# Kernel optimization log

Measured on AMD Instinct MI355X. Metric: run time of the kernel, lower is better.

The kernel has to match this reference:

```python
import jax, jax.numpy as jnp
import numpy as np
import math

AVGF = 16  # num_submatrices
TK = 4     # num_blocks
HA = 16    # num_heads
M = 2048   # M_size1 = C1*C2 = 32*64
DH = M // HA
EPS = 1e-5


def _layernorm(y, g, b):
    m = y.mean(-1, keepdims=True)
    v = ((y - m) ** 2).mean(-1, keepdims=True)
    return (y - m) / jnp.sqrt(v + EPS) * g + b


def setup_inputs() -> dict:
    key = jax.random.key(0)
    ks = jax.random.split(key, 10)
    f32 = jnp.float32
    return {
        "x": jax.random.normal(ks[0], (64, 32, 160), dtype=f32),
        "weight": jax.random.normal(ks[1], (M, M), dtype=f32),
        "bias": 0.02 * jax.random.normal(ks[2], (AVGF + 1, M), dtype=f32),
        "cls": 0.02 * jax.random.normal(ks[3], (1, M), dtype=f32),
        "Wqkv": jax.random.normal(ks[4], (TK, 3, HA, DH, M), dtype=f32),
        "Wo": jax.random.normal(ks[5], (TK, M, M), dtype=f32),
        "ln1_g": jnp.ones((M,), f32), "ln1_b": jnp.zeros((M,), f32),
        "ln2_g": jnp.ones((M,), f32), "ln2_b": jnp.zeros((M,), f32),
        "ln3_g": jnp.ones((M,), f32), "ln3_b": jnp.zeros((M,), f32),
        "fc1_w": jax.random.normal(ks[6], (4 * M, M), dtype=f32) * 0.02,
        "fc1_b": jnp.zeros((4 * M,), f32),
        "fc2_w": jax.random.normal(ks[7], (M, 4 * M), dtype=f32) * 0.02,
        "fc2_b": jnp.zeros((M,), f32),
    }


def reference(x, weight, bias, cls, Wqkv, Wo, ln1_g, ln1_b, ln2_g, ln2_b,
              ln3_g, ln3_b, fc1_w, fc1_b, fc2_w, fc2_b):
    inp = jnp.transpose(x, (2, 1, 0))           # [T, C1, C2] = [160, 32, 64]
    T, C1, C2 = inp.shape
    seg = T // AVGF
    # segment-average then flatten: [avgf, M]
    altx = inp.reshape(AVGF, seg, C1 * C2).mean(axis=1)
    savespace = jnp.einsum('lm,im->il', weight, altx)     # [avgf, M]
    savespace = jnp.concatenate([cls, savespace], axis=0) + bias  # [avgf+1, M]
    scale = 1.0 / math.sqrt(DH)

    def block(ss, params):
        Wqkv_a, Wo_a = params
        qkv = jnp.einsum('xhdm,im->xihd', Wqkv_a, _layernorm(ss, ln1_g, ln1_b))
        q, k, v = qkv[0], qkv[1], qkv[2]        # [avgf+1, hA, Dh]
        rsa = jnp.einsum('ihd,ihd->ih', q * scale, k)
        imv = rsa[..., None] * v                # [avgf+1, hA, Dh]
        # original loop: subj in 1..avgf-1  => cumsum over rows 0..avgf-1,
        # last row (index avgf) left untouched
        imv = jnp.concatenate([jnp.cumsum(imv[:AVGF], axis=0), imv[AVGF:]], axis=0)
        ss = imv.reshape(AVGF + 1, M) @ Wo_a.T + ss
        h = _layernorm(ss, ln2_g, ln2_b)
        h = jax.nn.gelu(h @ fc1_w.T + fc1_b, approximate=False) @ fc2_w.T + fc2_b
        return h + ss, None

    savespace, _ = jax.lax.scan(block, savespace, (Wqkv, Wo))
    out = _layernorm(savespace, ln3_g, ln3_b)
    return out.reshape(AVGF + 1, C1, C2)
```

## Files before the change

kernel.cpp:

```cpp
#include <hip/hip_runtime.h>
#include <math.h>


__global__ void k0_init(const float* __restrict__ x,
                        const float* __restrict__ bias,
                        const float* __restrict__ cls,
                        float* __restrict__ ss,
                        float* __restrict__ altx) {
    int idx = blockIdx.x * 256 + threadIdx.x;
    if (idx < 17 * 2048) {
        int r = idx >> 11, m = idx & 2047;
        float v = bias[idx];
        if (r == 0) v += cls[m];
        ss[idx] = v;
    }
    if (idx < 16 * 2048) {
        int i = idx >> 11, m = idx & 2047;
        int c1 = m >> 6, c2 = m & 63;
        const float* p = x + (size_t)(c2 * 32 + c1) * 160 + i * 10;
        float s = 0.f;
#pragma unroll
        for (int j = 0; j < 10; ++j) s += p[j];
        altx[idx] = s * 0.1f;
    }
}

template <int NR>
__global__ __launch_bounds__(256) void gemmS(
    const float* __restrict__ W, const float* __restrict__ act,
    float* __restrict__ P, int L, int K) {
    const int lane = threadIdx.x & 63;
    const int wv = threadIdx.x >> 6;
    const int l0 = blockIdx.x * 16 + wv * 4;
    const int slab = K / gridDim.y;
    const int k0 = blockIdx.y * slab;

    float acc[NR][4];
#pragma unroll
    for (int i = 0; i < NR; ++i)
#pragma unroll
        for (int r = 0; r < 4; ++r) acc[i][r] = 0.f;

    const float* Wp = W + (size_t)l0 * K + k0;
    const float* Ap = act + k0;

    for (int kk = 0; kk < slab; kk += 256) {
        const int idx = kk + lane * 4;
        const float4 w40 = *reinterpret_cast<const float4*>(Wp + idx);
        const float4 w41 = *reinterpret_cast<const float4*>(Wp + (size_t)K + idx);
        const float4 w42 = *reinterpret_cast<const float4*>(Wp + (size_t)2 * K + idx);
        const float4 w43 = *reinterpret_cast<const float4*>(Wp + (size_t)3 * K + idx);
#pragma unroll
        for (int i = 0; i < NR; ++i) {
            const float4 a4 = *reinterpret_cast<const float4*>(Ap + (size_t)i * K + idx);
            acc[i][0] += a4.x * w40.x + a4.y * w40.y + a4.z * w40.z + a4.w * w40.w;
            acc[i][1] += a4.x * w41.x + a4.y * w41.y + a4.z * w41.z + a4.w * w41.w;
            acc[i][2] += a4.x * w42.x + a4.y * w42.y + a4.z * w42.z + a4.w * w42.w;
            acc[i][3] += a4.x * w43.x + a4.y * w43.y + a4.z * w43.z + a4.w * w43.w;
        }
    }
    float vout = 0.f, vout2 = 0.f;
#pragma unroll
    for (int i = 0; i < NR; ++i)
#pragma unroll
        for (int r = 0; r < 4; ++r) {
            float v = acc[i][r];
#pragma unroll
            for (int off = 32; off; off >>= 1) v += __shfl_xor(v, off);
            if (i < 16) { if (lane == i * 4 + r) vout = v; }
            else        { if (lane == r)         vout2 = v; }
        }
    size_t pb = (size_t)blockIdx.y * NR * L + l0;
    P[pb + (size_t)(lane >> 2) * L + (lane & 3)] = vout;
    if (NR > 16 && lane < 4) P[pb + (size_t)16 * L + lane] = vout2;
}

__global__ void red_plain(const float* __restrict__ P, float* __restrict__ out,
                          int S, int NRL) {
    int idx = blockIdx.x * 256 + threadIdx.x;
    float s = 0.f;
    for (int y = 0; y < S; ++y) s += P[(size_t)y * NRL + idx];
    out[idx] = s;
}

__global__ void red_gelu(const float* __restrict__ P, const float* __restrict__ fb,
                         float* __restrict__ out, int S, int NRL) {
    int idx = blockIdx.x * 256 + threadIdx.x;
    float s = fb[idx & 8191];
    for (int y = 0; y < S; ++y) s += P[(size_t)y * NRL + idx];
    out[idx] = 0.5f * s * (1.f + erff(s * 0.70710678f));
}

__global__ void redln(const float* __restrict__ P, int S, int rowoff, int NRL,
                      const float* __restrict__ fb, float* __restrict__ ss,
                      const float* __restrict__ g, const float* __restrict__ b,
                      float* __restrict__ lnout) {
    const int row = blockIdx.x;
    const int tid = threadIdx.x;
    const int base = row * 2048;
    float vv[8];
    float s = 0.f, q = 0.f;
#pragma unroll
    for (int c = 0; c < 8; ++c) {
        int col = tid + c * 256;
        float xv = ss[base + col];
        if (row >= rowoff) {
            const float* pp = P + (size_t)(row - rowoff) * 2048 + col;
            for (int y = 0; y < S; ++y) xv += pp[(size_t)y * NRL];
        }
        if (fb != nullptr) xv += fb[col];
        ss[base + col] = xv;
        vv[c] = xv;
        s += xv;
        q += xv * xv;
    }
#pragma unroll
    for (int off = 32; off; off >>= 1) {
        s += __shfl_xor(s, off);
        q += __shfl_xor(q, off);
    }
    __shared__ float red[8];
    int wv = tid >> 6;
    if ((tid & 63) == 0) { red[wv] = s; red[4 + wv] = q; }
    __syncthreads();
    s = red[0] + red[1] + red[2] + red[3];
    q = red[4] + red[5] + red[6] + red[7];
    float mean = s * (1.f / 2048.f);
    float var = q * (1.f / 2048.f) - mean * mean;
    float rstd = rsqrtf(var + 1e-5f);
#pragma unroll
    for (int c = 0; c < 8; ++c) {
        int col = tid + c * 256;
        lnout[base + col] = (vv[c] - mean) * rstd * g[col] + b[col];
    }
}

__global__ void attn_kernel(const float* __restrict__ qkv, float* __restrict__ imv) {
    int h = blockIdx.x, lane = threadIdx.x;
    const float scale = 0.08838834764831845f;
    float run0 = 0.f, run1 = 0.f;
    for (int i = 0; i < 17; ++i) {
        const float* base = qkv + (size_t)i * 6144 + h * 128;
        float q0 = base[lane], q1 = base[lane + 64];
        float k0 = base[2048 + lane], k1 = base[2048 + lane + 64];
        float v0 = base[4096 + lane], v1 = base[4096 + lane + 64];
        float p = q0 * k0 + q1 * k1;
#pragma unroll
        for (int off = 32; off; off >>= 1) p += __shfl_xor(p, off);
        float rsa = p * scale;
        float iv0 = rsa * v0, iv1 = rsa * v1;
        float o0, o1;
        if (i < 16) { run0 += iv0; run1 += iv1; o0 = run0; o1 = run1; }
        else        { o0 = iv0; o1 = iv1; }
        imv[(size_t)i * 2048 + h * 128 + lane] = o0;
        imv[(size_t)i * 2048 + h * 128 + lane + 64] = o1;
    }
}

extern "C" void kernel_launch(void* const* d_in, const int* in_sizes, int n_in,
                              void* d_out, int out_size, void* d_ws, size_t ws_size,
                              hipStream_t stream) {
    const float* x      = (const float*)d_in[0];
    const float* weight = (const float*)d_in[1];
    const float* bias   = (const float*)d_in[2];
    const float* cls    = (const float*)d_in[3];
    const float* Wqkv   = (const float*)d_in[4];
    const float* Wo     = (const float*)d_in[5];
    const float* ln1_g  = (const float*)d_in[6];
    const float* ln1_b  = (const float*)d_in[7];
    const float* ln2_g  = (const float*)d_in[8];
    const float* ln2_b  = (const float*)d_in[9];
    const float* ln3_g  = (const float*)d_in[10];
    const float* ln3_b  = (const float*)d_in[11];
    const float* fc1_w  = (const float*)d_in[12];
    const float* fc1_b  = (const float*)d_in[13];
    const float* fc2_w  = (const float*)d_in[14];
    const float* fc2_b  = (const float*)d_in[15];
    float* out = (float*)d_out;

    float* ws     = (float*)d_ws;
    float* ss     = ws;
    float* altx   = ws + 34816;
    float* qkv    = ws + 67584;
    float* imv    = ws + 172032;
    float* tbuf   = ws + 206848;
    float* ln1buf = ws + 346112;
    float* ln2buf = ws + 380928;
    float* P      = ws + 415744;

    k0_init<<<136, 256, 0, stream>>>(x, bias, cls, ss, altx);
    gemmS<16><<<dim3(128, 4), 256, 0, stream>>>(weight, altx, P, 2048, 2048);
    redln<<<17, 256, 0, stream>>>(P, 4, 1, 32768, nullptr, ss, ln1_g, ln1_b, ln1buf);

    for (int k = 0; k < 4; ++k) {
        gemmS<17><<<dim3(384, 2), 256, 0, stream>>>(
            Wqkv + (size_t)k * 12582912, ln1buf, P, 6144, 2048);
        red_plain<<<408, 256, 0, stream>>>(P, qkv, 2, 104448);
        attn_kernel<<<16, 64, 0, stream>>>(qkv, imv);
        gemmS<17><<<dim3(128, 4), 256, 0, stream>>>(
            Wo + (size_t)k * 4194304, imv, P, 2048, 2048);
        redln<<<17, 256, 0, stream>>>(P, 4, 0, 34816, nullptr, ss, ln2_g, ln2_b, ln2buf);
        gemmS<17><<<dim3(512, 2), 256, 0, stream>>>(fc1_w, ln2buf, P, 8192, 2048);
        red_gelu<<<544, 256, 0, stream>>>(P, fc1_b, tbuf, 2, 139264);
        gemmS<17><<<dim3(128, 8), 256, 0, stream>>>(fc2_w, tbuf, P, 2048, 8192);
        if (k < 3)
            redln<<<17, 256, 0, stream>>>(P, 8, 0, 34816, fc2_b, ss, ln1_g, ln1_b, ln1buf);
        else
            redln<<<17, 256, 0, stream>>>(P, 8, 0, 34816, fc2_b, ss, ln3_g, ln3_b, out);
    }
}
```

Measured before the change: 580.7 us.

## Fuse layernorm, split-K reductions and GELU into GEMM activation staging

```diff
diff --git a/kernel.cpp b/kernel.cpp
--- a/kernel.cpp
+++ b/kernel.cpp
@@ -25,76 +25,98 @@
     }
 }
 
-template <int NR>
-__global__ __launch_bounds__(256) void gemmS(
+template <int NR, int MODE>
+__global__ __launch_bounds__(256) void gemmL(
     const float* __restrict__ W, const float* __restrict__ act,
-    float* __restrict__ P, int L, int K) {
-    const int lane = threadIdx.x & 63;
-    const int wv = threadIdx.x >> 6;
+    const float* __restrict__ st, const float* __restrict__ g,
+    const float* __restrict__ b, float* __restrict__ P,
+    int L, int K, int SP, int ANRL) {
+    __shared__ float abuf[NR][512];
+    const int tid = threadIdx.x;
+    const int lane = tid & 63;
+    const int qg = lane >> 4;
+    const int tl = lane & 15;
+    const int wv = tid >> 6;
     const int l0 = blockIdx.x * 16 + wv * 4;
-    const int slab = K / gridDim.y;
-    const int k0 = blockIdx.y * slab;
-
-    float acc[NR][4];
-#pragma unroll
-    for (int i = 0; i < NR; ++i)
-#pragma unroll
-        for (int r = 0; r < 4; ++r) acc[i][r] = 0.f;
-
-    const float* Wp = W + (size_t)l0 * K + k0;
-    const float* Ap = act + k0;
-
-    for (int kk = 0; kk < slab; kk += 256) {
-        const int idx = kk + lane * 4;
-        const float4 w40 = *reinterpret_cast<const float4*>(Wp + idx);
-        const float4 w41 = *reinterpret_cast<const float4*>(Wp + (size_t)K + idx);
-        const float4 w42 = *reinterpret_cast<const float4*>(Wp + (size_t)2 * K + idx);
-        const float4 w43 = *reinterpret_cast<const float4*>(Wp + (size_t)3 * K + idx);
-#pragma unroll
-        for (int i = 0; i < NR; ++i) {
-            const float4 a4 = *reinterpret_cast<const float4*>(Ap + (size_t)i * K + idx);
-            acc[i][0] += a4.x * w40.x + a4.y * w40.y + a4.z * w40.z + a4.w * w40.w;
-            acc[i][1] += a4.x * w41.x + a4.y * w41.y + a4.z * w41.z + a4.w * w41.w;
-            acc[i][2] += a4.x * w42.x + a4.y * w42.y + a4.z * w42.z + a4.w * w42.w;
-            acc[i][3] += a4.x * w43.x + a4.y * w43.y + a4.z * w43.z + a4.w * w43.w;
-        }
-    }
-    float vout = 0.f, vout2 = 0.f;
-#pragma unroll
-    for (int i = 0; i < NR; ++i)
-#pragma unroll
-        for (int r = 0; r < 4; ++r) {
-            float v = acc[i][r];
-#pragma unroll
-            for (int off = 32; off; off >>= 1) v += __shfl_xor(v, off);
-            if (i < 16) { if (lane == i * 4 + r) vout = v; }
-            else        { if (lane == r)         vout2 = v; }
-        }
-    size_t pb = (size_t)blockIdx.y * NR * L + l0;
-    P[pb + (size_t)(lane >> 2) * L + (lane & 3)] = vout;
-    if (NR > 16 && lane < 4) P[pb + (size_t)16 * L + lane] = vout2;
-}
-
-__global__ void red_plain(const float* __restrict__ P, float* __restrict__ out,
-                          int S, int NRL) {
-    int idx = blockIdx.x * 256 + threadIdx.x;
-    float s = 0.f;
-    for (int y = 0; y < S; ++y) s += P[(size_t)y * NRL + idx];
-    out[idx] = s;
-}
-
-__global__ void red_gelu(const float* __restrict__ P, const float* __restrict__ fb,
-                         float* __restrict__ out, int S, int NRL) {
-    int idx = blockIdx.x * 256 + threadIdx.x;
-    float s = fb[idx & 8191];
-    for (int y = 0; y < S; ++y) s += P[(size_t)y * NRL + idx];
-    out[idx] = 0.5f * s * (1.f + erff(s * 0.70710678f));
+    const int k0 = blockIdx.y * 512;
+
+    for (int e = tid; e < NR * 128; e += 256) {
+        const int i = e >> 7, c4 = e & 127;
+        const int m = k0 + c4 * 4;
+        float4 v4;
+        if (MODE == 2) {
+            v4 = *reinterpret_cast<const float4*>(act + (size_t)i * K + m);
+            for (int s = 1; s < SP; ++s) {
+                const float4 p4 = *reinterpret_cast<const float4*>(
+                    act + (size_t)s * ANRL + (size_t)i * K + m);
+                v4.x += p4.x; v4.y += p4.y; v4.z += p4.z; v4.w += p4.w;
+            }
+            const float4 b4 = *reinterpret_cast<const float4*>(b + m);
+            v4.x += b4.x; v4.y += b4.y; v4.z += b4.z; v4.w += b4.w;
+            v4.x = 0.5f * v4.x * (1.f + erff(v4.x * 0.70710678f));
+            v4.y = 0.5f * v4.y * (1.f + erff(v4.y * 0.70710678f));
+            v4.z = 0.5f * v4.z * (1.f + erff(v4.z * 0.70710678f));
+            v4.w = 0.5f * v4.w * (1.f + erff(v4.w * 0.70710678f));
+        } else {
+            v4 = *reinterpret_cast<const float4*>(act + (size_t)i * K + m);
+            if (MODE == 1) {
+                const float mean = st[2 * i], rstd = st[2 * i + 1];
+                const float4 g4 = *reinterpret_cast<const float4*>(g + m);
+                const float4 b4 = *reinterpret_cast<const float4*>(b + m);
+                v4.x = (v4.x - mean) * rstd * g4.x + b4.x;
+                v4.y = (v4.y - mean) * rstd * g4.y + b4.y;
+                v4.z = (v4.z - mean) * rstd * g4.z + b4.z;
+                v4.w = (v4.w - mean) * rstd * g4.w + b4.w;
+            }
+        }
+        *reinterpret_cast<float4*>(&abuf[i][c4 * 4]) = v4;
+    }
+    __syncthreads();
+
+    const float* Wrow = W + (size_t)(l0 + qg) * K + k0;
+    float4 w[8];
+#pragma unroll
+    for (int c = 0; c < 2; ++c)
+#pragma unroll
+        for (int s = 0; s < 4; ++s)
+            w[c * 4 + s] = *reinterpret_cast<const float4*>(
+                Wrow + c * 256 + s * 64 + tl * 4);
+
+    float acc[NR];
+#pragma unroll
+    for (int i = 0; i < NR; ++i) acc[i] = 0.f;
+
+#pragma unroll
+    for (int c = 0; c < 2; ++c)
+#pragma unroll
+        for (int s = 0; s < 4; ++s) {
+            const int off = c * 256 + s * 64 + tl * 4;
+            const float4 w4 = w[c * 4 + s];
+#pragma unroll
+            for (int i = 0; i < NR; ++i) {
+                const float4 a4 = *reinterpret_cast<const float4*>(&abuf[i][off]);
+                acc[i] += a4.x * w4.x + a4.y * w4.y + a4.z * w4.z + a4.w * w4.w;
+            }
+        }
+
+#pragma unroll
+    for (int i = 0; i < NR; ++i) {
+#pragma unroll
+        for (int off = 8; off; off >>= 1) acc[i] += __shfl_xor(acc[i], off);
+    }
+    float vout = acc[0];
+#pragma unroll
+    for (int i = 1; i < 16; ++i)
+        if (i < NR && tl == i) vout = acc[i];
+    const size_t pb = (size_t)blockIdx.y * NR * L + l0 + qg;
+    if (tl < NR) P[pb + (size_t)tl * L] = vout;
+    if (NR > 16 && tl == 0) P[pb + (size_t)16 * L] = acc[16];
 }
 
 __global__ void redln(const float* __restrict__ P, int S, int rowoff, int NRL,
                       const float* __restrict__ fb, float* __restrict__ ss,
-                      const float* __restrict__ g, const float* __restrict__ b,
-                      float* __restrict__ lnout) {
+                      float* __restrict__ st, const float* __restrict__ g,
+                      const float* __restrict__ b, float* __restrict__ lnout) {
     const int row = blockIdx.x;
     const int tid = threadIdx.x;
     const int base = row * 2048;
@@ -120,30 +142,38 @@
         q += __shfl_xor(q, off);
     }
     __shared__ float red[8];
-    int wv = tid >> 6;
-    if ((tid & 63) == 0) { red[wv] = s; red[4 + wv] = q; }
+    int wvi = tid >> 6;
+    if ((tid & 63) == 0) { red[wvi] = s; red[4 + wvi] = q; }
     __syncthreads();
     s = red[0] + red[1] + red[2] + red[3];
     q = red[4] + red[5] + red[6] + red[7];
     float mean = s * (1.f / 2048.f);
     float var = q * (1.f / 2048.f) - mean * mean;
     float rstd = rsqrtf(var + 1e-5f);
-#pragma unroll
-    for (int c = 0; c < 8; ++c) {
-        int col = tid + c * 256;
-        lnout[base + col] = (vv[c] - mean) * rstd * g[col] + b[col];
-    }
-}
-
-__global__ void attn_kernel(const float* __restrict__ qkv, float* __restrict__ imv) {
+    if (tid == 0) { st[2 * row] = mean; st[2 * row + 1] = rstd; }
+    if (lnout != nullptr) {
+#pragma unroll
+        for (int c = 0; c < 8; ++c) {
+            int col = tid + c * 256;
+            lnout[base + col] = (vv[c] - mean) * rstd * g[col] + b[col];
+        }
+    }
+}
+
+__global__ void attn_kernel(const float* __restrict__ Pq, float* __restrict__ imv) {
     int h = blockIdx.x, lane = threadIdx.x;
     const float scale = 0.08838834764831845f;
     float run0 = 0.f, run1 = 0.f;
     for (int i = 0; i < 17; ++i) {
-        const float* base = qkv + (size_t)i * 6144 + h * 128;
-        float q0 = base[lane], q1 = base[lane + 64];
-        float k0 = base[2048 + lane], k1 = base[2048 + lane + 64];
-        float v0 = base[4096 + lane], v1 = base[4096 + lane + 64];
+        const size_t idx = (size_t)i * 6144 + h * 128;
+        float q0 = 0.f, q1 = 0.f, k0 = 0.f, k1 = 0.f, v0 = 0.f, v1 = 0.f;
+#pragma unroll
+        for (int s = 0; s < 4; ++s) {
+            const float* base = Pq + (size_t)s * 104448 + idx;
+            q0 += base[lane];        q1 += base[lane + 64];
+            k0 += base[2048 + lane]; k1 += base[2048 + lane + 64];
+            v0 += base[4096 + lane]; v1 += base[4096 + lane + 64];
+        }
         float p = q0 * k0 + q1 * k1;
 #pragma unroll
         for (int off = 32; off; off >>= 1) p += __shfl_xor(p, off);
@@ -178,34 +208,40 @@
     const float* fc2_b  = (const float*)d_in[15];
     float* out = (float*)d_out;
 
-    float* ws     = (float*)d_ws;
-    float* ss     = ws;
-    float* altx   = ws + 34816;
-    float* qkv    = ws + 67584;
-    float* imv    = ws + 172032;
-    float* tbuf   = ws + 206848;
-    float* ln1buf = ws + 346112;
-    float* ln2buf = ws + 380928;
-    float* P      = ws + 415744;
+    float* ws   = (float*)d_ws;
+    float* ss   = ws;
+    float* altx = ws + 34816;
+    float* imv  = ws + 67584;
+    float* st0  = ws + 102400;
+    float* st1  = ws + 102464;
+    float* Pa   = ws + 102528;
+    float* Pb   = ws + 659584;
 
     k0_init<<<136, 256, 0, stream>>>(x, bias, cls, ss, altx);
-    gemmS<16><<<dim3(128, 4), 256, 0, stream>>>(weight, altx, P, 2048, 2048);
-    redln<<<17, 256, 0, stream>>>(P, 4, 1, 32768, nullptr, ss, ln1_g, ln1_b, ln1buf);
+    gemmL<16, 0><<<dim3(128, 4), 256, 0, stream>>>(
+        weight, altx, nullptr, nullptr, nullptr, Pa, 2048, 2048, 0, 0);
+    redln<<<17, 256, 0, stream>>>(Pa, 4, 1, 32768, nullptr, ss, st0,
+                                  nullptr, nullptr, nullptr);
 
     for (int k = 0; k < 4; ++k) {
-        gemmS<17><<<dim3(384, 2), 256, 0, stream>>>(
-            Wqkv + (size_t)k * 12582912, ln1buf, P, 6144, 2048);
-        red_plain<<<408, 256, 0, stream>>>(P, qkv, 2, 104448);
-        attn_kernel<<<16, 64, 0, stream>>>(qkv, imv);
-        gemmS<17><<<dim3(128, 4), 256, 0, stream>>>(
-            Wo + (size_t)k * 4194304, imv, P, 2048, 2048);
-        redln<<<17, 256, 0, stream>>>(P, 4, 0, 34816, nullptr, ss, ln2_g, ln2_b, ln2buf);
-        gemmS<17><<<dim3(512, 2), 256, 0, stream>>>(fc1_w, ln2buf, P, 8192, 2048);
-        red_gelu<<<544, 256, 0, stream>>>(P, fc1_b, tbuf, 2, 139264);
-        gemmS<17><<<dim3(128, 8), 256, 0, stream>>>(fc2_w, tbuf, P, 2048, 8192);
+        gemmL<17, 1><<<dim3(384, 4), 256, 0, stream>>>(
+            Wqkv + (size_t)k * 12582912, ss, st0, ln1_g, ln1_b, Pa,
+            6144, 2048, 0, 0);
+        attn_kernel<<<16, 64, 0, stream>>>(Pa, imv);
+        gemmL<17, 0><<<dim3(128, 4), 256, 0, stream>>>(
+            Wo + (size_t)k * 4194304, imv, nullptr, nullptr, nullptr, Pa,
+            2048, 2048, 0, 0);
+        redln<<<17, 256, 0, stream>>>(Pa, 4, 0, 34816, nullptr, ss, st1,
+                                      nullptr, nullptr, nullptr);
+        gemmL<17, 1><<<dim3(512, 4), 256, 0, stream>>>(
+            fc1_w, ss, st1, ln2_g, ln2_b, Pa, 8192, 2048, 0, 0);
+        gemmL<17, 2><<<dim3(128, 16), 256, 0, stream>>>(
+            fc2_w, Pa, nullptr, nullptr, fc1_b, Pb, 2048, 8192, 4, 139264);
         if (k < 3)
-            redln<<<17, 256, 0, stream>>>(P, 8, 0, 34816, fc2_b, ss, ln1_g, ln1_b, ln1buf);
+            redln<<<17, 256, 0, stream>>>(Pb, 16, 0, 34816, fc2_b, ss, st0,
+                                          nullptr, nullptr, nullptr);
         else
-            redln<<<17, 256, 0, stream>>>(P, 8, 0, 34816, fc2_b, ss, ln3_g, ln3_b, out);
-    }
-}
+            redln<<<17, 256, 0, stream>>>(Pb, 16, 0, 34816, fc2_b, ss, st0,
+                                          ln3_g, ln3_b, out);
+    }
+}
```

Measured after the change: 756.5 us. 30.3% more time.

## Double-buffer activations in LDS and prefetch weights in skinny GEMM; fuse QKV reduction into attention

Applied to the files above, without the earlier changes.

```diff
diff --git a/kernel.cpp b/kernel.cpp
--- a/kernel.cpp
+++ b/kernel.cpp
@@ -26,14 +26,22 @@
 }
 
 template <int NR>
-__global__ __launch_bounds__(256) void gemmS(
+__global__ __launch_bounds__(256, 4) void gemmT(
     const float* __restrict__ W, const float* __restrict__ act,
-    float* __restrict__ P, int L, int K) {
-    const int lane = threadIdx.x & 63;
-    const int wv = threadIdx.x >> 6;
+    float* __restrict__ P, int L, int K, int NC) {
+    __shared__ float abuf[2][NR][256];
+    const int tid = threadIdx.x;
+    const int lane = tid & 63;
+    const int wv = tid >> 6;
     const int l0 = blockIdx.x * 16 + wv * 4;
-    const int slab = K / gridDim.y;
-    const int k0 = blockIdx.y * slab;
+    const int k0 = blockIdx.y * (NC << 8);
+
+    for (int i = wv; i < NR; i += 4)
+        __builtin_amdgcn_global_load_lds(
+            (const __attribute__((address_space(1))) unsigned int*)
+                (act + (size_t)i * K + k0 + lane * 4),
+            (__attribute__((address_space(3))) unsigned int*)(&abuf[0][i][0]),
+            16, 0, 0);
 
     float acc[NR][4];
 #pragma unroll
@@ -41,24 +49,44 @@
 #pragma unroll
         for (int r = 0; r < 4; ++r) acc[i][r] = 0.f;
 
-    const float* Wp = W + (size_t)l0 * K + k0;
-    const float* Ap = act + k0;
-
-    for (int kk = 0; kk < slab; kk += 256) {
-        const int idx = kk + lane * 4;
-        const float4 w40 = *reinterpret_cast<const float4*>(Wp + idx);
-        const float4 w41 = *reinterpret_cast<const float4*>(Wp + (size_t)K + idx);
-        const float4 w42 = *reinterpret_cast<const float4*>(Wp + (size_t)2 * K + idx);
-        const float4 w43 = *reinterpret_cast<const float4*>(Wp + (size_t)3 * K + idx);
+    const float* Wbase = W + (size_t)l0 * K + k0;
+    float4 wp[4], wn[4];
+#pragma unroll
+    for (int r = 0; r < 4; ++r)
+        wp[r] = *reinterpret_cast<const float4*>(Wbase + (size_t)r * K + lane * 4);
+#pragma unroll
+    for (int r = 0; r < 4; ++r) wn[r] = wp[r];
+
+    __syncthreads();
+
+    for (int c = 0; c < NC; ++c) {
+        if (c + 1 < NC) {
+            for (int i = wv; i < NR; i += 4)
+                __builtin_amdgcn_global_load_lds(
+                    (const __attribute__((address_space(1))) unsigned int*)
+                        (act + (size_t)i * K + k0 + (c + 1) * 256 + lane * 4),
+                    (__attribute__((address_space(3))) unsigned int*)
+                        (&abuf[(c + 1) & 1][i][0]),
+                    16, 0, 0);
+#pragma unroll
+            for (int r = 0; r < 4; ++r)
+                wn[r] = *reinterpret_cast<const float4*>(
+                    Wbase + (size_t)r * K + (c + 1) * 256 + lane * 4);
+        }
+        const float* ab = &abuf[c & 1][0][0];
 #pragma unroll
         for (int i = 0; i < NR; ++i) {
-            const float4 a4 = *reinterpret_cast<const float4*>(Ap + (size_t)i * K + idx);
-            acc[i][0] += a4.x * w40.x + a4.y * w40.y + a4.z * w40.z + a4.w * w40.w;
-            acc[i][1] += a4.x * w41.x + a4.y * w41.y + a4.z * w41.z + a4.w * w41.w;
-            acc[i][2] += a4.x * w42.x + a4.y * w42.y + a4.z * w42.z + a4.w * w42.w;
-            acc[i][3] += a4.x * w43.x + a4.y * w43.y + a4.z * w43.z + a4.w * w43.w;
-        }
-    }
+            const float4 a4 = *reinterpret_cast<const float4*>(ab + i * 256 + lane * 4);
+            acc[i][0] += a4.x * wp[0].x + a4.y * wp[0].y + a4.z * wp[0].z + a4.w * wp[0].w;
+            acc[i][1] += a4.x * wp[1].x + a4.y * wp[1].y + a4.z * wp[1].z + a4.w * wp[1].w;
+            acc[i][2] += a4.x * wp[2].x + a4.y * wp[2].y + a4.z * wp[2].z + a4.w * wp[2].w;
+            acc[i][3] += a4.x * wp[3].x + a4.y * wp[3].y + a4.z * wp[3].z + a4.w * wp[3].w;
+        }
+        __syncthreads();
+#pragma unroll
+        for (int r = 0; r < 4; ++r) wp[r] = wn[r];
+    }
+
     float vout = 0.f, vout2 = 0.f;
 #pragma unroll
     for (int i = 0; i < NR; ++i)
@@ -70,17 +98,9 @@
             if (i < 16) { if (lane == i * 4 + r) vout = v; }
             else        { if (lane == r)         vout2 = v; }
         }
-    size_t pb = (size_t)blockIdx.y * NR * L + l0;
+    const size_t pb = (size_t)blockIdx.y * NR * L + l0;
     P[pb + (size_t)(lane >> 2) * L + (lane & 3)] = vout;
     if (NR > 16 && lane < 4) P[pb + (size_t)16 * L + lane] = vout2;
-}
-
-__global__ void red_plain(const float* __restrict__ P, float* __restrict__ out,
-                          int S, int NRL) {
-    int idx = blockIdx.x * 256 + threadIdx.x;
-    float s = 0.f;
-    for (int y = 0; y < S; ++y) s += P[(size_t)y * NRL + idx];
-    out[idx] = s;
 }
 
 __global__ void red_gelu(const float* __restrict__ P, const float* __restrict__ fb,
@@ -120,8 +140,8 @@
         q += __shfl_xor(q, off);
     }
     __shared__ float red[8];
-    int wv = tid >> 6;
-    if ((tid & 63) == 0) { red[wv] = s; red[4 + wv] = q; }
+    int wvi = tid >> 6;
+    if ((tid & 63) == 0) { red[wvi] = s; red[4 + wvi] = q; }
     __syncthreads();
     s = red[0] + red[1] + red[2] + red[3];
     q = red[4] + red[5] + red[6] + red[7];
@@ -135,15 +155,20 @@
     }
 }
 
-__global__ void attn_kernel(const float* __restrict__ qkv, float* __restrict__ imv) {
+__global__ void attn_kernel(const float* __restrict__ Pq, float* __restrict__ imv) {
     int h = blockIdx.x, lane = threadIdx.x;
     const float scale = 0.08838834764831845f;
     float run0 = 0.f, run1 = 0.f;
     for (int i = 0; i < 17; ++i) {
-        const float* base = qkv + (size_t)i * 6144 + h * 128;
-        float q0 = base[lane], q1 = base[lane + 64];
-        float k0 = base[2048 + lane], k1 = base[2048 + lane + 64];
-        float v0 = base[4096 + lane], v1 = base[4096 + lane + 64];
+        const size_t idx = (size_t)i * 6144 + h * 128;
+        float q0 = 0.f, q1 = 0.f, k0 = 0.f, k1 = 0.f, v0 = 0.f, v1 = 0.f;
+#pragma unroll
+        for (int s = 0; s < 4; ++s) {
+            const float* base = Pq + (size_t)s * 104448 + idx;
+            q0 += base[lane];        q1 += base[lane + 64];
+            k0 += base[2048 + lane]; k1 += base[2048 + lane + 64];
+            v0 += base[4096 + lane]; v1 += base[4096 + lane + 64];
+        }
         float p = q0 * k0 + q1 * k1;
 #pragma unroll
         for (int off = 32; off; off >>= 1) p += __shfl_xor(p, off);
@@ -181,28 +206,26 @@
     float* ws     = (float*)d_ws;
     float* ss     = ws;
     float* altx   = ws + 34816;
-    float* qkv    = ws + 67584;
-    float* imv    = ws + 172032;
-    float* tbuf   = ws + 206848;
-    float* ln1buf = ws + 346112;
-    float* ln2buf = ws + 380928;
-    float* P      = ws + 415744;
+    float* imv    = ws + 67584;
+    float* tbuf   = ws + 102400;
+    float* ln1buf = ws + 241664;
+    float* ln2buf = ws + 276480;
+    float* P      = ws + 311296;
 
     k0_init<<<136, 256, 0, stream>>>(x, bias, cls, ss, altx);
-    gemmS<16><<<dim3(128, 4), 256, 0, stream>>>(weight, altx, P, 2048, 2048);
+    gemmT<16><<<dim3(128, 4), 256, 0, stream>>>(weight, altx, P, 2048, 2048, 2);
     redln<<<17, 256, 0, stream>>>(P, 4, 1, 32768, nullptr, ss, ln1_g, ln1_b, ln1buf);
 
     for (int k = 0; k < 4; ++k) {
-        gemmS<17><<<dim3(384, 2), 256, 0, stream>>>(
-            Wqkv + (size_t)k * 12582912, ln1buf, P, 6144, 2048);
-        red_plain<<<408, 256, 0, stream>>>(P, qkv, 2, 104448);
-        attn_kernel<<<16, 64, 0, stream>>>(qkv, imv);
-        gemmS<17><<<dim3(128, 4), 256, 0, stream>>>(
-            Wo + (size_t)k * 4194304, imv, P, 2048, 2048);
+        gemmT<17><<<dim3(384, 4), 256, 0, stream>>>(
+            Wqkv + (size_t)k * 12582912, ln1buf, P, 6144, 2048, 2);
+        attn_kernel<<<16, 64, 0, stream>>>(P, imv);
+        gemmT<17><<<dim3(128, 4), 256, 0, stream>>>(
+            Wo + (size_t)k * 4194304, imv, P, 2048, 2048, 2);
         redln<<<17, 256, 0, stream>>>(P, 4, 0, 34816, nullptr, ss, ln2_g, ln2_b, ln2buf);
-        gemmS<17><<<dim3(512, 2), 256, 0, stream>>>(fc1_w, ln2buf, P, 8192, 2048);
+        gemmT<17><<<dim3(512, 2), 256, 0, stream>>>(fc1_w, ln2buf, P, 8192, 2048, 4);
         red_gelu<<<544, 256, 0, stream>>>(P, fc1_b, tbuf, 2, 139264);
-        gemmS<17><<<dim3(128, 8), 256, 0, stream>>>(fc2_w, tbuf, P, 2048, 8192);
+        gemmT<17><<<dim3(128, 8), 256, 0, stream>>>(fc2_w, tbuf, P, 2048, 8192, 4);
         if (k < 3)
             redln<<<17, 256, 0, stream>>>(P, 8, 0, 34816, fc2_b, ss, ln1_g, ln1_b, ln1buf);
         else
```

Result: slower. 686.3 us (+18.2%).

## Restructure skinny GEMM: 4 output cols per block, rows split across waves, prefetch

Applied to the files above, without the earlier changes.

```diff
diff --git a/kernel.cpp b/kernel.cpp
--- a/kernel.cpp
+++ b/kernel.cpp
@@ -26,68 +26,68 @@
 }
 
 template <int NR>
-__global__ __launch_bounds__(256) void gemmS(
+__global__ __launch_bounds__(256, 4) void gemvP(
     const float* __restrict__ W, const float* __restrict__ act,
     float* __restrict__ P, int L, int K) {
     const int lane = threadIdx.x & 63;
-    const int wv = threadIdx.x >> 6;
-    const int l0 = blockIdx.x * 16 + wv * 4;
-    const int slab = K / gridDim.y;
-    const int k0 = blockIdx.y * slab;
-
-    float acc[NR][4];
-#pragma unroll
-    for (int i = 0; i < NR; ++i)
-#pragma unroll
-        for (int r = 0; r < 4; ++r) acc[i][r] = 0.f;
-
-    const float* Wp = W + (size_t)l0 * K + k0;
-    const float* Ap = act + k0;
-
-    for (int kk = 0; kk < slab; kk += 256) {
-        const int idx = kk + lane * 4;
-        const float4 w40 = *reinterpret_cast<const float4*>(Wp + idx);
-        const float4 w41 = *reinterpret_cast<const float4*>(Wp + (size_t)K + idx);
-        const float4 w42 = *reinterpret_cast<const float4*>(Wp + (size_t)2 * K + idx);
-        const float4 w43 = *reinterpret_cast<const float4*>(Wp + (size_t)3 * K + idx);
-#pragma unroll
-        for (int i = 0; i < NR; ++i) {
-            const float4 a4 = *reinterpret_cast<const float4*>(Ap + (size_t)i * K + idx);
-            acc[i][0] += a4.x * w40.x + a4.y * w40.y + a4.z * w40.z + a4.w * w40.w;
-            acc[i][1] += a4.x * w41.x + a4.y * w41.y + a4.z * w41.z + a4.w * w41.w;
-            acc[i][2] += a4.x * w42.x + a4.y * w42.y + a4.z * w42.z + a4.w * w42.w;
-            acc[i][3] += a4.x * w43.x + a4.y * w43.y + a4.z * w43.z + a4.w * w43.w;
+    const int qt = threadIdx.x >> 6;
+    const int I0 = (qt * 4 < NR - 5) ? qt * 4 : NR - 5;
+    const int l0 = blockIdx.x * 4;
+    const int k0 = blockIdx.y * 2048;
+    const float* Wp = W + (size_t)l0 * K + k0 + lane * 4;
+    const float* Ap = act + (size_t)I0 * K + k0 + lane * 4;
+
+    float acc[5][4];
+#pragma unroll
+    for (int j = 0; j < 5; ++j)
+#pragma unroll
+        for (int r = 0; r < 4; ++r) acc[j][r] = 0.f;
+
+    float4 w4[4], wn[4];
+#pragma unroll
+    for (int r = 0; r < 4; ++r)
+        w4[r] = *reinterpret_cast<const float4*>(Wp + (size_t)r * K);
+
+    for (int c = 0; c < 8; ++c) {
+        float4 a4[5];
+#pragma unroll
+        for (int j = 0; j < 5; ++j)
+            a4[j] = *reinterpret_cast<const float4*>(Ap + (size_t)j * K + c * 256);
+        if (c < 7) {
+#pragma unroll
+            for (int r = 0; r < 4; ++r)
+                wn[r] = *reinterpret_cast<const float4*>(
+                    Wp + (size_t)r * K + (c + 1) * 256);
         }
-    }
-    float vout = 0.f, vout2 = 0.f;
-#pragma unroll
-    for (int i = 0; i < NR; ++i)
+#pragma unroll
+        for (int j = 0; j < 5; ++j)
+#pragma unroll
+            for (int r = 0; r < 4; ++r)
+                acc[j][r] += a4[j].x * w4[r].x + a4[j].y * w4[r].y +
+                             a4[j].z * w4[r].z + a4[j].w * w4[r].w;
+#pragma unroll
+        for (int r = 0; r < 4; ++r) w4[r] = wn[r];
+    }
+
+    float vout = 0.f;
+#pragma unroll
+    for (int j = 0; j < 5; ++j)
 #pragma unroll
         for (int r = 0; r < 4; ++r) {
-            float v = acc[i][r];
+            float v = acc[j][r];
 #pragma unroll
             for (int off = 32; off; off >>= 1) v += __shfl_xor(v, off);
-            if (i < 16) { if (lane == i * 4 + r) vout = v; }
-            else        { if (lane == r)         vout2 = v; }
+            if (lane == j * 4 + r) vout = v;
         }
-    size_t pb = (size_t)blockIdx.y * NR * L + l0;
-    P[pb + (size_t)(lane >> 2) * L + (lane & 3)] = vout;
-    if (NR > 16 && lane < 4) P[pb + (size_t)16 * L + lane] = vout2;
-}
-
-__global__ void red_plain(const float* __restrict__ P, float* __restrict__ out,
-                          int S, int NRL) {
+    if (lane < 20)
+        P[(size_t)blockIdx.y * NR * L + (size_t)(I0 + (lane >> 2)) * L +
+          l0 + (lane & 3)] = vout;
+}
+
+__global__ void red_gelu(const float* __restrict__ Pf, const float* __restrict__ fb,
+                         float* __restrict__ out) {
     int idx = blockIdx.x * 256 + threadIdx.x;
-    float s = 0.f;
-    for (int y = 0; y < S; ++y) s += P[(size_t)y * NRL + idx];
-    out[idx] = s;
-}
-
-__global__ void red_gelu(const float* __restrict__ P, const float* __restrict__ fb,
-                         float* __restrict__ out, int S, int NRL) {
-    int idx = blockIdx.x * 256 + threadIdx.x;
-    float s = fb[idx & 8191];
-    for (int y = 0; y < S; ++y) s += P[(size_t)y * NRL + idx];
+    float s = fb[idx & 8191] + Pf[idx];
     out[idx] = 0.5f * s * (1.f + erff(s * 0.70710678f));
 }
 
@@ -120,8 +120,8 @@
         q += __shfl_xor(q, off);
     }
     __shared__ float red[8];
-    int wv = tid >> 6;
-    if ((tid & 63) == 0) { red[wv] = s; red[4 + wv] = q; }
+    int wvi = tid >> 6;
+    if ((tid & 63) == 0) { red[wvi] = s; red[4 + wvi] = q; }
     __syncthreads();
     s = red[0] + red[1] + red[2] + red[3];
     q = red[4] + red[5] + red[6] + red[7];
@@ -181,31 +181,31 @@
     float* ws     = (float*)d_ws;
     float* ss     = ws;
     float* altx   = ws + 34816;
-    float* qkv    = ws + 67584;
-    float* imv    = ws + 172032;
-    float* tbuf   = ws + 206848;
-    float* ln1buf = ws + 346112;
-    float* ln2buf = ws + 380928;
-    float* P      = ws + 415744;
+    float* imv    = ws + 67584;
+    float* qkv    = ws + 102400;
+    float* Pf     = ws + 206848;
+    float* tbuf   = ws + 346112;
+    float* ln1buf = ws + 485376;
+    float* ln2buf = ws + 520192;
+    float* Pg     = ws + 555008;
 
     k0_init<<<136, 256, 0, stream>>>(x, bias, cls, ss, altx);
-    gemmS<16><<<dim3(128, 4), 256, 0, stream>>>(weight, altx, P, 2048, 2048);
-    redln<<<17, 256, 0, stream>>>(P, 4, 1, 32768, nullptr, ss, ln1_g, ln1_b, ln1buf);
+    gemvP<16><<<dim3(512, 1), 256, 0, stream>>>(weight, altx, Pg, 2048, 2048);
+    redln<<<17, 256, 0, stream>>>(Pg, 1, 1, 32768, nullptr, ss, ln1_g, ln1_b, ln1buf);
 
     for (int k = 0; k < 4; ++k) {
-        gemmS<17><<<dim3(384, 2), 256, 0, stream>>>(
-            Wqkv + (size_t)k * 12582912, ln1buf, P, 6144, 2048);
-        red_plain<<<408, 256, 0, stream>>>(P, qkv, 2, 104448);
+        gemvP<17><<<dim3(1536, 1), 256, 0, stream>>>(
+            Wqkv + (size_t)k * 12582912, ln1buf, qkv, 6144, 2048);
         attn_kernel<<<16, 64, 0, stream>>>(qkv, imv);
-        gemmS<17><<<dim3(128, 4), 256, 0, stream>>>(
-            Wo + (size_t)k * 4194304, imv, P, 2048, 2048);
-        redln<<<17, 256, 0, stream>>>(P, 4, 0, 34816, nullptr, ss, ln2_g, ln2_b, ln2buf);
-        gemmS<17><<<dim3(512, 2), 256, 0, stream>>>(fc1_w, ln2buf, P, 8192, 2048);
-        red_gelu<<<544, 256, 0, stream>>>(P, fc1_b, tbuf, 2, 139264);
-        gemmS<17><<<dim3(128, 8), 256, 0, stream>>>(fc2_w, tbuf, P, 2048, 8192);
+        gemvP<17><<<dim3(512, 1), 256, 0, stream>>>(
+            Wo + (size_t)k * 4194304, imv, Pg, 2048, 2048);
+        redln<<<17, 256, 0, stream>>>(Pg, 1, 0, 34816, nullptr, ss, ln2_g, ln2_b, ln2buf);
+        gemvP<17><<<dim3(2048, 1), 256, 0, stream>>>(fc1_w, ln2buf, Pf, 8192, 2048);
+        red_gelu<<<544, 256, 0, stream>>>(Pf, fc1_b, tbuf);
+        gemvP<17><<<dim3(512, 4), 256, 0, stream>>>(fc2_w, tbuf, Pg, 2048, 8192);
         if (k < 3)
-            redln<<<17, 256, 0, stream>>>(P, 8, 0, 34816, fc2_b, ss, ln1_g, ln1_b, ln1buf);
+            redln<<<17, 256, 0, stream>>>(Pg, 4, 0, 34816, fc2_b, ss, ln1_g, ln1_b, ln1buf);
         else
-            redln<<<17, 256, 0, stream>>>(P, 8, 0, 34816, fc2_b, ss, ln3_g, ln3_b, out);
-    }
-}
+            redln<<<17, 256, 0, stream>>>(Pg, 4, 0, 34816, fc2_b, ss, ln3_g, ln3_b, out);
+    }
+}
```

After: 503.1 us. 1.15x faster.
